# Kernel tuning notes

Measured on AMD Instinct MI355X. Metric: run time of the kernel, lower is better.

Reference implementation:

```python
import jax, jax.numpy as jnp
import numpy as np

B, N, D, H, NC = 4, 32, 128, 8, 27
DK = D // H
DFF = 4 * D
L = NC * N


def layer_norm(x, g, b, eps=1e-5):
    mu = jnp.mean(x, -1, keepdims=True)
    var = jnp.var(x, -1, keepdims=True)
    return (x - mu) * jax.lax.rsqrt(var + eps) * g + b


def setup_inputs() -> dict:
    ks = jax.random.split(jax.random.key(0), 16)
    s = 1.0 / np.sqrt(D)
    return {
        'x': jax.random.normal(ks[0], (B, N, D), jnp.float32),
        'mask': jax.random.randint(ks[1], (B, 1, N), 0, 2, jnp.int32),
        'coords': jax.random.normal(ks[2], (B, NC, N, 3), jnp.float32),
        'Wp': jax.random.normal(ks[3], (3, D), jnp.float32) * 0.5,
        'bp': jnp.zeros((D,), jnp.float32),
        'Wq': jax.random.normal(ks[4], (D, D), jnp.float32) * s,
        'bq': jnp.zeros((D,), jnp.float32),
        'Wk': jax.random.normal(ks[5], (D, D), jnp.float32) * s,
        'bk': jnp.zeros((D,), jnp.float32),
        'Wv': jax.random.normal(ks[6], (D, D), jnp.float32) * s,
        'bv': jnp.zeros((D,), jnp.float32),
        'Wo': jax.random.normal(ks[7], (D, D), jnp.float32) * s,
        'bo': jnp.zeros((D,), jnp.float32),
        'g1': jnp.ones((D,), jnp.float32),
        'b1': jnp.zeros((D,), jnp.float32),
        'g2': jnp.ones((D,), jnp.float32),
        'b2': jnp.zeros((D,), jnp.float32),
        'W1': jax.random.normal(ks[8], (D, DFF), jnp.float32) * s,
        'bf1': jnp.zeros((DFF,), jnp.float32),
        'W2': jax.random.normal(ks[9], (DFF, D), jnp.float32) * (1.0 / np.sqrt(DFF)),
        'bf2': jnp.zeros((D,), jnp.float32),
    }


def reference(x, mask, coords, Wp, bp, Wq, bq, Wk, bk, Wv, bv, Wo, bo,
              g1, b1, g2, b2, W1, bf1, W2, bf2):
    mask_enh = jnp.tile(mask, (1, NC, 1)).reshape(B, 1, 1, L)

    def step(i):
        # position_encoding: x broadcast over 27 images + linear of coords relative to atom i
        ci = jax.lax.dynamic_slice_in_dim(coords, i, 1, axis=2)        # [B,NC,1,3]
        ar = x[:, None] + (coords - ci) @ Wp + bp                      # [B,NC,N,D]
        a = ar.reshape(B, L, D)
        hn = layer_norm(a, g1, b1)
        q = (hn @ Wq + bq).reshape(B, L, H, DK).transpose(0, 2, 1, 3)
        k = (hn @ Wk + bk).reshape(B, L, H, DK).transpose(0, 2, 1, 3)
        v = (hn @ Wv + bv).reshape(B, L, H, DK).transpose(0, 2, 1, 3)
        scores = jnp.einsum('bhqd,bhkd->bhqk', q, k) / np.sqrt(DK)     # [B,H,L,L]
        scores = jnp.where(mask_enh == 0, -1e9, scores)
        att = jnp.einsum('bhqk,bhkd->bhqd', jax.nn.softmax(scores, -1), v)
        att = att.transpose(0, 2, 1, 3).reshape(B, L, D) @ Wo + bo
        s = a + att  # SublayerConnection (dropout identity in eval)
        # original keeps only [b, image 0, atom i] of the [B,NC,N,D] reshape; flat index = i
        return jax.lax.dynamic_slice_in_dim(s, i, 1, axis=1)[:, 0]     # [B,D]

    rows = jax.lax.map(step, jnp.arange(N))                            # [N,B,D]
    y = rows.transpose(1, 0, 2)                                        # [B,N,D]
    hn2 = layer_norm(y, g2, b2)
    return y + (jax.nn.relu(hn2 @ W1 + bf1) @ W2 + bf2)
```

## Files before the change

### kernel.cpp

```cpp
#include <hip/hip_runtime.h>


#define B_ 4
#define N_ 32
#define D_ 128
#define H_ 8
#define NC_ 27
#define DFF_ 512
#define L_ (NC_*N_)

__device__ __forceinline__ float wred(float v){
  #pragma unroll
  for (int off = 32; off; off >>= 1) v += __shfl_xor(v, off);
  return v;
}

__global__ __launch_bounds__(1024) void k_fused(
    const float* __restrict__ x, const int* __restrict__ mask,
    const float* __restrict__ coords,
    const float* __restrict__ Wp, const float* __restrict__ bp,
    const float* __restrict__ Wq, const float* __restrict__ bq,
    const float* __restrict__ Wk, const float* __restrict__ bk,
    const float* __restrict__ Wv, const float* __restrict__ bv,
    const float* __restrict__ Wo, const float* __restrict__ bo,
    const float* __restrict__ g1, const float* __restrict__ b1,
    const float* __restrict__ g2, const float* __restrict__ b2,
    const float* __restrict__ W1, const float* __restrict__ bf1,
    const float* __restrict__ W2, const float* __restrict__ bfb2,
    float* __restrict__ out)
{
  __shared__ float sc_s[H_*L_];
  __shared__ float is_s[L_];
  __shared__ float dc_s[3][L_];
  __shared__ float xg_s[N_][D_+1];
  __shared__ float zz_s[H_][D_+1];
  __shared__ float w_s[3][D_];
  __shared__ float wcg_s[3][D_];
  __shared__ float g1_s[D_], b1_s[D_], bp_s[D_], bq_s[D_], bk_s[D_];
  __shared__ float g2_s[D_], b2_s[D_], bv_s[D_], bo_s[D_], bfb2_s[D_];
  __shared__ float q_s[D_], hn_s[D_], hn2_s[D_], att_s[D_], y_s[D_];
  __shared__ float qAxk_s[H_][N_];
  __shared__ float qGk_s[H_][3];
  __shared__ float S3_s[H_];
  __shared__ float varx_s[N_];
  __shared__ float dxp_s[N_][3];
  __shared__ int   mask_s[N_];
  __shared__ float cq_s[NC_][3];
  __shared__ float M6_s[6], mwp_s[3], P6_s[6];
  __shared__ float pmax_s[H_][2];
  __shared__ float Tnp_s[H_][2][N_];
  __shared__ float Sp_s[H_][2], RDp_s[H_][2][3];
  __shared__ float f_s[DFF_];
  __shared__ float po[8][D_];

  int bi = blockIdx.x;
  int b = bi >> 5, i = bi & 31;
  int tid = threadIdx.x, wave = tid >> 6, lane = tid & 63;

  int r0 = wave*2, r1 = wave*2+1;
  float xa0 = x[(size_t)(b*N_+r0)*D_ + lane];
  float xa1 = x[(size_t)(b*N_+r0)*D_ + lane+64];
  float xb0 = x[(size_t)(b*N_+r1)*D_ + lane];
  float xb1 = x[(size_t)(b*N_+r1)*D_ + lane+64];
  float xi0 = 0.f, xi1 = 0.f;
  if (wave == 0){ xi0 = x[(size_t)bi*D_+lane]; xi1 = x[(size_t)bi*D_+lane+64]; }
  float ck0=0.f, ck1=0.f, ck2=0.f;
  if (tid < L_){
    int c = tid >> 5, n = tid & 31;
    const float* ck = coords + ((size_t)(b*NC_+c)*N_ + n)*3;
    ck0 = ck[0]; ck1 = ck[1]; ck2 = ck[2];
  }
  if (tid < 384) w_s[tid>>7][tid&127] = Wp[tid];
  if (tid < 128)                g2_s[tid]       = g2[tid];
  else if (tid < 256)           b2_s[tid-128]   = b2[tid-128];
  else if (tid < 384)           bv_s[tid-256]   = bv[tid-256];
  else if (tid < 512){ int t=tid-384; g1_s[t]=g1[t]; bo_s[t]=bo[t]; }
  else if (tid < 640){ int t=tid-512; b1_s[t]=b1[t]; bfb2_s[t]=bfb2[t]; }
  else if (tid < 768){ int t=tid-640; bp_s[t]=bp[t]; bq_s[t]=bq[t]; }
  else if (tid < 800)           mask_s[tid-768] = mask[b*N_ + (tid-768)];
  else if (tid < 881){
    int t = tid-800;
    cq_s[t/3][t%3] = coords[((size_t)(b*NC_ + t/3)*N_ + i)*3 + t%3];
  }
  else if (tid < 1009)          bk_s[tid-881]   = bk[tid-881];
  __syncthreads();

  {
    float t0 = xa0 + bp_s[lane], t1 = xa1 + bp_s[lane+64];
    float mean = wred(t0+t1)*(1.f/D_);
    float h0 = t0-mean, h1 = t1-mean;
    xg_s[r0][lane]    = h0*g1_s[lane];
    xg_s[r0][lane+64] = h1*g1_s[lane+64];
    float vv = h0*h0 + h1*h1;
    float d0 = h0*w_s[0][lane] + h1*w_s[0][lane+64];
    float d1 = h0*w_s[1][lane] + h1*w_s[1][lane+64];
    float d2 = h0*w_s[2][lane] + h1*w_s[2][lane+64];
    #pragma unroll
    for (int off=32; off; off>>=1){
      vv += __shfl_xor(vv,off); d0 += __shfl_xor(d0,off);
      d1 += __shfl_xor(d1,off); d2 += __shfl_xor(d2,off);
    }
    if (lane==0){ varx_s[r0]=vv*(1.f/D_);
      dxp_s[r0][0]=d0; dxp_s[r0][1]=d1; dxp_s[r0][2]=d2; }
    t0 = xb0 + bp_s[lane]; t1 = xb1 + bp_s[lane+64];
    mean = wred(t0+t1)*(1.f/D_);
    h0 = t0-mean; h1 = t1-mean;
    xg_s[r1][lane]    = h0*g1_s[lane];
    xg_s[r1][lane+64] = h1*g1_s[lane+64];
    vv = h0*h0 + h1*h1;
    d0 = h0*w_s[0][lane] + h1*w_s[0][lane+64];
    d1 = h0*w_s[1][lane] + h1*w_s[1][lane+64];
    d2 = h0*w_s[2][lane] + h1*w_s[2][lane+64];
    #pragma unroll
    for (int off=32; off; off>>=1){
      vv += __shfl_xor(vv,off); d0 += __shfl_xor(d0,off);
      d1 += __shfl_xor(d1,off); d2 += __shfl_xor(d2,off);
    }
    if (lane==0){ varx_s[r1]=vv*(1.f/D_);
      dxp_s[r1][0]=d0; dxp_s[r1][1]=d1; dxp_s[r1][2]=d2; }
  }
  float dc0=0.f, dc1=0.f, dc2=0.f;
  if (tid < L_){
    int c = tid >> 5;
    dc0 = ck0 - cq_s[c][0]; dc1 = ck1 - cq_s[c][1]; dc2 = ck2 - cq_s[c][2];
    dc_s[0][tid]=dc0; dc_s[1][tid]=dc1; dc_s[2][tid]=dc2;
  }
  if (wave >= 8 && wave < 11){
    int j = wave - 8;
    float s = w_s[j][lane] + w_s[j][lane+64];
    s = wred(s);
    if (lane==0) mwp_s[j] = s*(1.f/D_);
  }
  if (wave >= 10){
    int idx = wave - 10;
    int ja = (idx>=3) + (idx>=5);
    int jb = idx - (idx>=3)*2 - (idx>=5);
    float s = w_s[ja][lane]*w_s[jb][lane] + w_s[ja][lane+64]*w_s[jb][lane+64];
    s = wred(s);
    if (lane==0) P6_s[idx] = s;
  }
  __syncthreads();

  if (tid < 384){ int j=tid>>7, e=tid&127;
    wcg_s[j][e] = (w_s[j][e] - mwp_s[j])*g1_s[e]; }
  if (tid == 384){
    M6_s[0]=P6_s[0]-D_*mwp_s[0]*mwp_s[0];
    M6_s[1]=P6_s[1]-D_*mwp_s[0]*mwp_s[1];
    M6_s[2]=P6_s[2]-D_*mwp_s[0]*mwp_s[2];
    M6_s[3]=P6_s[3]-D_*mwp_s[1]*mwp_s[1];
    M6_s[4]=P6_s[4]-D_*mwp_s[1]*mwp_s[2];
    M6_s[5]=P6_s[5]-D_*mwp_s[2]*mwp_s[2];
  }
  if (tid >= 512 && tid < 640){ int e = tid-512;
    hn_s[e] = xg_s[i][e]*rsqrtf(varx_s[i]+1e-5f) + b1_s[e]; }
  __syncthreads();

  {
    int slot = tid>>7, d = tid&127;
    float a = 0.f;
    #pragma unroll
    for (int e = slot*16; e < slot*16+16; e++) a += hn_s[e]*Wq[e*D_+d];
    po[slot][d] = a;
  }
  __syncthreads();

  if (tid < D_){
    float a = bq_s[tid];
    #pragma unroll
    for (int s=0;s<8;s++) a += po[s][tid];
    q_s[tid] = a;
  }
  __syncthreads();

  {
    int h = tid>>7, e = tid&127;
    const float4* wk4 = (const float4*)(Wk + (size_t)e*D_ + h*16);
    float s = 0.f;
    #pragma unroll
    for (int kq=0; kq<4; kq++){
      float4 w4 = wk4[kq];
      s += w4.x*q_s[h*16+kq*4+0] + w4.y*q_s[h*16+kq*4+1]
         + w4.z*q_s[h*16+kq*4+2] + w4.w*q_s[h*16+kq*4+3];
    }
    zz_s[h][e] = s;
  }
  __syncthreads();

  {
    int quarter = tid>>8, id = tid&255, h = id>>5, n = id&31;
    float s = 0.f;
    #pragma unroll 8
    for (int e = quarter*32; e < quarter*32+32; e++) s += xg_s[n][e]*zz_s[h][e];
    ((float*)po)[quarter*256 + id] = s;
  }
  __syncthreads();

  if (tid < 256){
    int h = tid>>5, n = tid&31;
    qAxk_s[h][n] = ((float*)po)[tid] + ((float*)po)[256+tid]
                 + ((float*)po)[512+tid] + ((float*)po)[768+tid];
  }
  if (wave >= 8){
    int h = wave - 8;
    float u0 = zz_s[h][lane], u1 = zz_s[h][lane+64];
    float s3 = b1_s[lane]*u0 + b1_s[lane+64]*u1;
    if (lane < 16) s3 += q_s[h*16+lane]*bk_s[h*16+lane];
    float qg0 = wcg_s[0][lane]*u0 + wcg_s[0][lane+64]*u1;
    float qg1 = wcg_s[1][lane]*u0 + wcg_s[1][lane+64]*u1;
    float qg2 = wcg_s[2][lane]*u0 + wcg_s[2][lane+64]*u1;
    #pragma unroll
    for (int off=32; off; off>>=1){
      s3  += __shfl_xor(s3,off);  qg0 += __shfl_xor(qg0,off);
      qg1 += __shfl_xor(qg1,off); qg2 += __shfl_xor(qg2,off);
    }
    if (lane==0){ S3_s[h]=s3; qGk_s[h][0]=qg0; qGk_s[h][1]=qg1; qGk_s[h][2]=qg2; }
  }
  __syncthreads();

  if (tid < L_){
    int n = tid & 31;
    float quad = dc0*dc0*M6_s[0] + dc1*dc1*M6_s[3] + dc2*dc2*M6_s[5]
               + 2.f*(dc0*dc1*M6_s[1] + dc0*dc2*M6_s[2] + dc1*dc2*M6_s[4]);
    float lin  = dc0*dxp_s[n][0] + dc1*dxp_s[n][1] + dc2*dxp_s[n][2];
    float E = varx_s[n] + (quad + 2.f*lin)*(1.f/D_);
    float is = rsqrtf(fmaxf(E, 0.f) + 1e-5f);
    is_s[tid] = is;
    bool mk = mask_s[n] != 0;
    #pragma unroll
    for (int h=0; h<H_; h++){
      float sc = 0.25f*(is*(qAxk_s[h][n]
               + dc0*qGk_s[h][0] + dc1*qGk_s[h][1] + dc2*qGk_s[h][2]) + S3_s[h]);
      sc_s[h*L_ + tid] = mk ? sc : -1e9f;
    }
  }
  __syncthreads();

  int h2 = wave>>1, sub = wave&1, n2 = lane&31, half2 = lane>>5;
  int q4 = sub*2 + half2, c0 = q4*7, c1 = (q4==3) ? NC_ : c0+7;
  {
    float M = -3.0e38f;
    for (int c=c0; c<c1; c++) M = fmaxf(M, sc_s[h2*L_ + c*N_ + n2]);
    #pragma unroll
    for (int off=32; off; off>>=1) M = fmaxf(M, __shfl_xor(M, off));
    if (lane==0) pmax_s[h2][sub] = M;
  }
  __syncthreads();

  {
    float M = fmaxf(pmax_s[h2][0], pmax_s[h2][1]);
    float S=0.f, Tn=0.f, rr0=0.f, rr1=0.f, rr2=0.f;
    for (int c=c0; c<c1; c++){
      int l = c*N_ + n2;
      float w_ = __expf(sc_s[h2*L_ + l] - M);
      float t = w_ * is_s[l];
      S += w_; Tn += t;
      rr0 += t*dc_s[0][l]; rr1 += t*dc_s[1][l]; rr2 += t*dc_s[2][l];
    }
    float Tn2 = Tn + __shfl_xor(Tn, 32);
    if (lane < 32) Tnp_s[h2][sub][lane] = Tn2;
    #pragma unroll
    for (int off=32; off; off>>=1){
      S   += __shfl_xor(S,off);   rr0 += __shfl_xor(rr0,off);
      rr1 += __shfl_xor(rr1,off); rr2 += __shfl_xor(rr2,off);
    }
    if (lane==0){ Sp_s[h2][sub]=S;
      RDp_s[h2][sub][0]=rr0; RDp_s[h2][sub][1]=rr1; RDp_s[h2][sub][2]=rr2; }
  }
  __syncthreads();

  {
    int h = tid>>7, e = tid&127;
    float rS = 1.f / fmaxf(Sp_s[h][0]+Sp_s[h][1], 1e-30f);
    float z = 0.f;
    #pragma unroll 8
    for (int n=0; n<N_; n++){
      float Tn = Tnp_s[h][0][n] + Tnp_s[h][1][n];
      z += Tn * xg_s[n][e];
    }
    float R0 = RDp_s[h][0][0]+RDp_s[h][1][0];
    float R1 = RDp_s[h][0][1]+RDp_s[h][1][1];
    float R2 = RDp_s[h][0][2]+RDp_s[h][1][2];
    z += R0*wcg_s[0][e] + R1*wcg_s[1][e] + R2*wcg_s[2][e];
    zz_s[h][e] = z*rS + b1_s[e];
  }
  __syncthreads();

  {
    int slot = tid>>7, d = tid&127, h = d>>4;
    float a = 0.f;
    #pragma unroll
    for (int e = slot*16; e < slot*16+16; e++) a += zz_s[h][e]*Wv[e*D_+d];
    po[slot][d] = a;
  }
  __syncthreads();

  if (tid < D_){
    float a = bv_s[tid];
    #pragma unroll
    for (int s=0;s<8;s++) a += po[s][tid];
    att_s[tid] = a;
  }
  __syncthreads();

  {
    int slot = tid>>7, d = tid&127;
    float a = 0.f;
    #pragma unroll
    for (int e = slot*16; e < slot*16+16; e++) a += att_s[e]*Wo[e*D_+d];
    po[slot][d] = a;
  }
  __syncthreads();

  if (wave == 0){
    float y0 = xi0 + bp_s[lane]    + bo_s[lane];
    float y1 = xi1 + bp_s[lane+64] + bo_s[lane+64];
    #pragma unroll
    for (int s=0;s<8;s++){ y0 += po[s][lane]; y1 += po[s][lane+64]; }
    y_s[lane] = y0; y_s[lane+64] = y1;
    float mean = wred(y0+y1)*(1.f/D_);
    float v0 = y0-mean, v1 = y1-mean;
    float var = wred(v0*v0+v1*v1)*(1.f/D_);
    float isd = rsqrtf(var + 1e-5f);
    hn2_s[lane]    = v0*isd*g2_s[lane]    + b2_s[lane];
    hn2_s[lane+64] = v1*isd*g2_s[lane+64] + b2_s[lane+64];
  }
  __syncthreads();

  {
    int col = tid&511, half = tid>>9;
    float a = half ? 0.f : bf1[col];
    #pragma unroll 16
    for (int e = half*64; e < half*64+64; e++)
      a += hn2_s[e]*W1[(size_t)e*DFF_ + col];
    ((float*)po)[tid] = a;
  }
  __syncthreads();

  if (tid < DFF_)
    f_s[tid] = fmaxf(((float*)po)[tid] + ((float*)po)[DFF_+tid], 0.f);
  __syncthreads();

  {
    int slot = tid>>7, d = tid&127;
    float a = 0.f;
    #pragma unroll 16
    for (int j = slot*64; j < slot*64+64; j++)
      a += f_s[j]*W2[(size_t)j*D_ + d];
    po[slot][d] = a;
  }
  __syncthreads();

  if (tid < D_){
    float a = y_s[tid] + bfb2_s[tid];
    #pragma unroll
    for (int s=0;s<8;s++) a += po[s][tid];
    out[(size_t)bi*D_ + tid] = a;
  }
}

extern "C" void kernel_launch(void* const* d_in, const int* in_sizes, int n_in,
                              void* d_out, int out_size, void* d_ws, size_t ws_size,
                              hipStream_t stream){
  const float* x      = (const float*)d_in[0];
  const int*   mask   = (const int*)  d_in[1];
  const float* coords = (const float*)d_in[2];
  const float* Wp     = (const float*)d_in[3];
  const float* bp     = (const float*)d_in[4];
  const float* Wq     = (const float*)d_in[5];
  const float* bq     = (const float*)d_in[6];
  const float* Wk     = (const float*)d_in[7];
  const float* bk     = (const float*)d_in[8];
  const float* Wv     = (const float*)d_in[9];
  const float* bv     = (const float*)d_in[10];
  const float* Wo     = (const float*)d_in[11];
  const float* bo     = (const float*)d_in[12];
  const float* g1     = (const float*)d_in[13];
  const float* b1     = (const float*)d_in[14];
  const float* g2     = (const float*)d_in[15];
  const float* b2     = (const float*)d_in[16];
  const float* W1     = (const float*)d_in[17];
  const float* bf1    = (const float*)d_in[18];
  const float* W2     = (const float*)d_in[19];
  const float* bfb2   = (const float*)d_in[20];

  k_fused<<<B_*N_, 1024, 0, stream>>>(x, mask, coords, Wp, bp, Wq, bq, Wk, bk,
                                      Wv, bv, Wo, bo, g1, b1, g2, b2,
                                      W1, bf1, W2, bfb2, (float*)d_out);
}
```

Before: 117.6 us.

## Prefetch weight tiles into registers as float4 and keep scores in registers

Weight slices for Wq, Wk, Wv, Wo, W1 and W2 are now loaded as float4 into registers early, ahead of the barriers before their use, so global latency overlaps earlier phases. The GEMV partial layout switches to 32 slices of 4 rows with a longer reduction. Attention scores are computed and kept in a per-thread register array, which drops the 27 KB score buffer in shared memory and one barrier; the inverse-std computation moves earlier and bf1 is staged in shared memory. The cost is much higher register pressure at 1024 threads per block (16 float4 for W1 and for W2) and longer partial-sum reductions.

```diff
diff --git a/kernel.cpp b/kernel.cpp
--- a/kernel.cpp
+++ b/kernel.cpp
@@ -29,7 +29,6 @@
     const float* __restrict__ W2, const float* __restrict__ bfb2,
     float* __restrict__ out)
 {
-  __shared__ float sc_s[H_*L_];
   __shared__ float is_s[L_];
   __shared__ float dc_s[3][L_];
   __shared__ float xg_s[N_][D_+1];
@@ -38,6 +37,7 @@
   __shared__ float wcg_s[3][D_];
   __shared__ float g1_s[D_], b1_s[D_], bp_s[D_], bq_s[D_], bk_s[D_];
   __shared__ float g2_s[D_], b2_s[D_], bv_s[D_], bo_s[D_], bfb2_s[D_];
+  __shared__ float bf1_s[DFF_];
   __shared__ float q_s[D_], hn_s[D_], hn2_s[D_], att_s[D_], y_s[D_];
   __shared__ float qAxk_s[H_][N_];
   __shared__ float qGk_s[H_][3];
@@ -46,16 +46,18 @@
   __shared__ float dxp_s[N_][3];
   __shared__ int   mask_s[N_];
   __shared__ float cq_s[NC_][3];
-  __shared__ float M6_s[6], mwp_s[3], P6_s[6];
+  __shared__ float mwp_s[3], P6_s[6];
   __shared__ float pmax_s[H_][2];
   __shared__ float Tnp_s[H_][2][N_];
   __shared__ float Sp_s[H_][2], RDp_s[H_][2][3];
   __shared__ float f_s[DFF_];
-  __shared__ float po[8][D_];
+  __shared__ float pf_s[4096];
+  float4* pf4 = (float4*)pf_s;
 
   int bi = blockIdx.x;
   int b = bi >> 5, i = bi & 31;
   int tid = threadIdx.x, wave = tid >> 6, lane = tid & 63;
+  int es = tid >> 5, d4 = tid & 31;
 
   int r0 = wave*2, r1 = wave*2+1;
   float xa0 = x[(size_t)(b*N_+r0)*D_ + lane];
@@ -70,19 +72,34 @@
     const float* ck = coords + ((size_t)(b*NC_+c)*N_ + n)*3;
     ck0 = ck[0]; ck1 = ck[1]; ck2 = ck[2];
   }
+  float4 wq4[4];
+  #pragma unroll
+  for (int k=0;k<4;k++)
+    wq4[k] = *(const float4*)(Wq + (size_t)(es*4+k)*D_ + d4*4);
+  float4 wk4[4];
+  {
+    int h = tid>>7, e = tid&127;
+    #pragma unroll
+    for (int k=0;k<4;k++)
+      wk4[k] = *(const float4*)(Wk + (size_t)e*D_ + h*16 + k*4);
+  }
   if (tid < 384) w_s[tid>>7][tid&127] = Wp[tid];
-  if (tid < 128)                g2_s[tid]       = g2[tid];
-  else if (tid < 256)           b2_s[tid-128]   = b2[tid-128];
-  else if (tid < 384)           bv_s[tid-256]   = bv[tid-256];
-  else if (tid < 512){ int t=tid-384; g1_s[t]=g1[t]; bo_s[t]=bo[t]; }
-  else if (tid < 640){ int t=tid-512; b1_s[t]=b1[t]; bfb2_s[t]=bfb2[t]; }
-  else if (tid < 768){ int t=tid-640; bp_s[t]=bp[t]; bq_s[t]=bq[t]; }
-  else if (tid < 800)           mask_s[tid-768] = mask[b*N_ + (tid-768)];
+  if      (tid < 128)  g1_s[tid]      = g1[tid];
+  else if (tid < 256)  b1_s[tid-128]  = b1[tid-128];
+  else if (tid < 384)  bp_s[tid-256]  = bp[tid-256];
+  else if (tid < 512)  bq_s[tid-384]  = bq[tid-384];
+  else if (tid < 640)  bk_s[tid-512]  = bk[tid-512];
+  else if (tid < 768)  g2_s[tid-640]  = g2[tid-640];
+  else if (tid < 896)  b2_s[tid-768]  = b2[tid-768];
+  else                 bv_s[tid-896]  = bv[tid-896];
+  if      (tid < 128)  bo_s[tid]      = bo[tid];
+  else if (tid < 256)  bfb2_s[tid-128]= bfb2[tid-128];
+  else if (tid < 768)  bf1_s[tid-256] = bf1[tid-256];
+  else if (tid < 800)  mask_s[tid-768]= mask[b*N_ + (tid-768)];
   else if (tid < 881){
     int t = tid-800;
     cq_s[t/3][t%3] = coords[((size_t)(b*NC_ + t/3)*N_ + i)*3 + t%3];
   }
-  else if (tid < 1009)          bk_s[tid-881]   = bk[tid-881];
   __syncthreads();
 
   {
@@ -141,46 +158,51 @@
   }
   __syncthreads();
 
+  if (tid < L_){
+    int n = tid & 31;
+    float m0 = mwp_s[0], m1 = mwp_s[1], m2 = mwp_s[2];
+    float M00 = P6_s[0]-D_*m0*m0, M01 = P6_s[1]-D_*m0*m1;
+    float M02 = P6_s[2]-D_*m0*m2, M11 = P6_s[3]-D_*m1*m1;
+    float M12 = P6_s[4]-D_*m1*m2, M22 = P6_s[5]-D_*m2*m2;
+    float quad = dc0*dc0*M00 + dc1*dc1*M11 + dc2*dc2*M22
+               + 2.f*(dc0*dc1*M01 + dc0*dc2*M02 + dc1*dc2*M12);
+    float lin  = dc0*dxp_s[n][0] + dc1*dxp_s[n][1] + dc2*dxp_s[n][2];
+    float E = varx_s[n] + (quad + 2.f*lin)*(1.f/D_);
+    is_s[tid] = rsqrtf(fmaxf(E, 0.f) + 1e-5f);
+  }
   if (tid < 384){ int j=tid>>7, e=tid&127;
     wcg_s[j][e] = (w_s[j][e] - mwp_s[j])*g1_s[e]; }
-  if (tid == 384){
-    M6_s[0]=P6_s[0]-D_*mwp_s[0]*mwp_s[0];
-    M6_s[1]=P6_s[1]-D_*mwp_s[0]*mwp_s[1];
-    M6_s[2]=P6_s[2]-D_*mwp_s[0]*mwp_s[2];
-    M6_s[3]=P6_s[3]-D_*mwp_s[1]*mwp_s[1];
-    M6_s[4]=P6_s[4]-D_*mwp_s[1]*mwp_s[2];
-    M6_s[5]=P6_s[5]-D_*mwp_s[2]*mwp_s[2];
-  }
-  if (tid >= 512 && tid < 640){ int e = tid-512;
+  if (tid >= 896){ int e = tid-896;
     hn_s[e] = xg_s[i][e]*rsqrtf(varx_s[i]+1e-5f) + b1_s[e]; }
   __syncthreads();
 
   {
-    int slot = tid>>7, d = tid&127;
-    float a = 0.f;
-    #pragma unroll
-    for (int e = slot*16; e < slot*16+16; e++) a += hn_s[e]*Wq[e*D_+d];
-    po[slot][d] = a;
+    float4 acc = {0.f,0.f,0.f,0.f};
+    #pragma unroll
+    for (int k=0;k<4;k++){
+      float h = hn_s[es*4+k];
+      acc.x += h*wq4[k].x; acc.y += h*wq4[k].y;
+      acc.z += h*wq4[k].z; acc.w += h*wq4[k].w;
+    }
+    pf4[es*32 + d4] = acc;
   }
   __syncthreads();
 
   if (tid < D_){
     float a = bq_s[tid];
     #pragma unroll
-    for (int s=0;s<8;s++) a += po[s][tid];
+    for (int s=0;s<32;s++) a += pf_s[s*D_+tid];
     q_s[tid] = a;
   }
   __syncthreads();
 
   {
     int h = tid>>7, e = tid&127;
-    const float4* wk4 = (const float4*)(Wk + (size_t)e*D_ + h*16);
     float s = 0.f;
     #pragma unroll
     for (int kq=0; kq<4; kq++){
-      float4 w4 = wk4[kq];
-      s += w4.x*q_s[h*16+kq*4+0] + w4.y*q_s[h*16+kq*4+1]
-         + w4.z*q_s[h*16+kq*4+2] + w4.w*q_s[h*16+kq*4+3];
+      s += wk4[kq].x*q_s[h*16+kq*4+0] + wk4[kq].y*q_s[h*16+kq*4+1]
+         + wk4[kq].z*q_s[h*16+kq*4+2] + wk4[kq].w*q_s[h*16+kq*4+3];
     }
     zz_s[h][e] = s;
   }
@@ -191,14 +213,13 @@
     float s = 0.f;
     #pragma unroll 8
     for (int e = quarter*32; e < quarter*32+32; e++) s += xg_s[n][e]*zz_s[h][e];
-    ((float*)po)[quarter*256 + id] = s;
+    pf_s[quarter*256 + id] = s;
   }
   __syncthreads();
 
   if (tid < 256){
-    int h = tid>>5, n = tid&31;
-    qAxk_s[h][n] = ((float*)po)[tid] + ((float*)po)[256+tid]
-                 + ((float*)po)[512+tid] + ((float*)po)[768+tid];
+    qAxk_s[tid>>5][tid&31] = pf_s[tid] + pf_s[256+tid]
+                           + pf_s[512+tid] + pf_s[768+tid];
   }
   if (wave >= 8){
     int h = wave - 8;
@@ -217,44 +238,49 @@
   }
   __syncthreads();
 
-  if (tid < L_){
-    int n = tid & 31;
-    float quad = dc0*dc0*M6_s[0] + dc1*dc1*M6_s[3] + dc2*dc2*M6_s[5]
-               + 2.f*(dc0*dc1*M6_s[1] + dc0*dc2*M6_s[2] + dc1*dc2*M6_s[4]);
-    float lin  = dc0*dxp_s[n][0] + dc1*dxp_s[n][1] + dc2*dxp_s[n][2];
-    float E = varx_s[n] + (quad + 2.f*lin)*(1.f/D_);
-    float is = rsqrtf(fmaxf(E, 0.f) + 1e-5f);
-    is_s[tid] = is;
-    bool mk = mask_s[n] != 0;
-    #pragma unroll
-    for (int h=0; h<H_; h++){
-      float sc = 0.25f*(is*(qAxk_s[h][n]
-               + dc0*qGk_s[h][0] + dc1*qGk_s[h][1] + dc2*qGk_s[h][2]) + S3_s[h]);
-      sc_s[h*L_ + tid] = mk ? sc : -1e9f;
-    }
-  }
-  __syncthreads();
-
   int h2 = wave>>1, sub = wave&1, n2 = lane&31, half2 = lane>>5;
   int q4 = sub*2 + half2, c0 = q4*7, c1 = (q4==3) ? NC_ : c0+7;
-  {
+  float sc[7];
+  {
+    float qa = qAxk_s[h2][n2];
+    float qg0 = qGk_s[h2][0], qg1 = qGk_s[h2][1], qg2 = qGk_s[h2][2];
+    float s3 = S3_s[h2];
+    bool mk = mask_s[n2] != 0;
     float M = -3.0e38f;
-    for (int c=c0; c<c1; c++) M = fmaxf(M, sc_s[h2*L_ + c*N_ + n2]);
+    #pragma unroll
+    for (int t=0; t<7; t++){
+      int c = c0+t;
+      if (c < c1){
+        int l = c*N_ + n2;
+        float v = 0.25f*(is_s[l]*(qa + dc_s[0][l]*qg0 + dc_s[1][l]*qg1
+                                     + dc_s[2][l]*qg2) + s3);
+        sc[t] = mk ? v : -1e9f;
+      } else sc[t] = -3.0e38f;
+      M = fmaxf(M, sc[t]);
+    }
     #pragma unroll
     for (int off=32; off; off>>=1) M = fmaxf(M, __shfl_xor(M, off));
     if (lane==0) pmax_s[h2][sub] = M;
   }
   __syncthreads();
 
+  float4 wv4[4];
+  #pragma unroll
+  for (int k=0;k<4;k++)
+    wv4[k] = *(const float4*)(Wv + (size_t)(es*4+k)*D_ + d4*4);
   {
     float M = fmaxf(pmax_s[h2][0], pmax_s[h2][1]);
     float S=0.f, Tn=0.f, rr0=0.f, rr1=0.f, rr2=0.f;
-    for (int c=c0; c<c1; c++){
-      int l = c*N_ + n2;
-      float w_ = __expf(sc_s[h2*L_ + l] - M);
-      float t = w_ * is_s[l];
-      S += w_; Tn += t;
-      rr0 += t*dc_s[0][l]; rr1 += t*dc_s[1][l]; rr2 += t*dc_s[2][l];
+    #pragma unroll
+    for (int t=0; t<7; t++){
+      int c = c0+t;
+      if (c < c1){
+        int l = c*N_ + n2;
+        float w_ = __expf(sc[t] - M);
+        float tt = w_ * is_s[l];
+        S += w_; Tn += tt;
+        rr0 += tt*dc_s[0][l]; rr1 += tt*dc_s[1][l]; rr2 += tt*dc_s[2][l];
+      }
     }
     float Tn2 = Tn + __shfl_xor(Tn, 32);
     if (lane < 32) Tnp_s[h2][sub][lane] = Tn2;
@@ -268,6 +294,10 @@
   }
   __syncthreads();
 
+  float4 wo4[4];
+  #pragma unroll
+  for (int k=0;k<4;k++)
+    wo4[k] = *(const float4*)(Wo + (size_t)(es*4+k)*D_ + d4*4);
   {
     int h = tid>>7, e = tid&127;
     float rS = 1.f / fmaxf(Sp_s[h][0]+Sp_s[h][1], 1e-30f);
@@ -286,36 +316,50 @@
   __syncthreads();
 
   {
-    int slot = tid>>7, d = tid&127, h = d>>4;
-    float a = 0.f;
-    #pragma unroll
-    for (int e = slot*16; e < slot*16+16; e++) a += zz_s[h][e]*Wv[e*D_+d];
-    po[slot][d] = a;
+    int h = d4 >> 2;
+    float4 acc = {0.f,0.f,0.f,0.f};
+    #pragma unroll
+    for (int k=0;k<4;k++){
+      float zv = zz_s[h][es*4+k];
+      acc.x += zv*wv4[k].x; acc.y += zv*wv4[k].y;
+      acc.z += zv*wv4[k].z; acc.w += zv*wv4[k].w;
+    }
+    pf4[es*32 + d4] = acc;
   }
   __syncthreads();
 
   if (tid < D_){
     float a = bv_s[tid];
     #pragma unroll
-    for (int s=0;s<8;s++) a += po[s][tid];
+    for (int s=0;s<32;s++) a += pf_s[s*D_+tid];
     att_s[tid] = a;
   }
   __syncthreads();
 
   {
-    int slot = tid>>7, d = tid&127;
-    float a = 0.f;
-    #pragma unroll
-    for (int e = slot*16; e < slot*16+16; e++) a += att_s[e]*Wo[e*D_+d];
-    po[slot][d] = a;
-  }
-  __syncthreads();
-
+    float4 acc = {0.f,0.f,0.f,0.f};
+    #pragma unroll
+    for (int k=0;k<4;k++){
+      float av = att_s[es*4+k];
+      acc.x += av*wo4[k].x; acc.y += av*wo4[k].y;
+      acc.z += av*wo4[k].z; acc.w += av*wo4[k].w;
+    }
+    pf4[es*32 + d4] = acc;
+  }
+  __syncthreads();
+
+  float4 w14[16];
+  {
+    int e8 = tid>>7, c4 = tid&127;
+    #pragma unroll
+    for (int k=0;k<16;k++)
+      w14[k] = *(const float4*)(W1 + (size_t)(e8*16+k)*DFF_ + c4*4);
+  }
   if (wave == 0){
     float y0 = xi0 + bp_s[lane]    + bo_s[lane];
     float y1 = xi1 + bp_s[lane+64] + bo_s[lane+64];
     #pragma unroll
-    for (int s=0;s<8;s++){ y0 += po[s][lane]; y1 += po[s][lane+64]; }
+    for (int s=0;s<32;s++){ y0 += pf_s[s*D_+lane]; y1 += pf_s[s*D_+lane+64]; }
     y_s[lane] = y0; y_s[lane+64] = y1;
     float mean = wred(y0+y1)*(1.f/D_);
     float v0 = y0-mean, v1 = y1-mean;
@@ -327,33 +371,50 @@
   __syncthreads();
 
   {
-    int col = tid&511, half = tid>>9;
-    float a = half ? 0.f : bf1[col];
-    #pragma unroll 16
-    for (int e = half*64; e < half*64+64; e++)
-      a += hn2_s[e]*W1[(size_t)e*DFF_ + col];
-    ((float*)po)[tid] = a;
-  }
-  __syncthreads();
-
-  if (tid < DFF_)
-    f_s[tid] = fmaxf(((float*)po)[tid] + ((float*)po)[DFF_+tid], 0.f);
-  __syncthreads();
-
-  {
-    int slot = tid>>7, d = tid&127;
-    float a = 0.f;
-    #pragma unroll 16
-    for (int j = slot*64; j < slot*64+64; j++)
-      a += f_s[j]*W2[(size_t)j*D_ + d];
-    po[slot][d] = a;
+    int e8 = tid>>7, c4 = tid&127;
+    float4 acc = {0.f,0.f,0.f,0.f};
+    #pragma unroll
+    for (int k=0;k<16;k++){
+      float h = hn2_s[e8*16+k];
+      acc.x += h*w14[k].x; acc.y += h*w14[k].y;
+      acc.z += h*w14[k].z; acc.w += h*w14[k].w;
+    }
+    pf4[e8*128 + c4] = acc;
+  }
+  __syncthreads();
+
+  float4 w24[16];
+  {
+    int js = tid>>5;
+    #pragma unroll
+    for (int k=0;k<16;k++)
+      w24[k] = *(const float4*)(W2 + (size_t)(js*16+k)*D_ + d4*4);
+  }
+  if (tid < DFF_){
+    float a = bf1_s[tid];
+    #pragma unroll
+    for (int s=0;s<8;s++) a += pf_s[s*DFF_+tid];
+    f_s[tid] = fmaxf(a, 0.f);
+  }
+  __syncthreads();
+
+  {
+    int js = tid>>5;
+    float4 acc = {0.f,0.f,0.f,0.f};
+    #pragma unroll
+    for (int k=0;k<16;k++){
+      float fv = f_s[js*16+k];
+      acc.x += fv*w24[k].x; acc.y += fv*w24[k].y;
+      acc.z += fv*w24[k].z; acc.w += fv*w24[k].w;
+    }
+    pf4[js*32 + d4] = acc;
   }
   __syncthreads();
 
   if (tid < D_){
     float a = y_s[tid] + bfb2_s[tid];
     #pragma unroll
-    for (int s=0;s<8;s++) a += po[s][tid];
+    for (int s=0;s<32;s++) a += pf_s[s*D_+tid];
     out[(size_t)bi*D_ + tid] = a;
   }
 }
```

New measurement: 112.5 us (median of 2 runs). 4.3% less time.
